# Performance work log

Hardware: AMD Instinct MI355X
Metric: run time of the kernel (lower is better)

Reference implementation:

```python
import jax, jax.numpy as jnp
import numpy as np
from jax import lax

K = 7            # neighborhood kernel size (odd)
HEADS = 6
DIM = 96
HID = int(DIM * 2.66)   # 255, Restormer-style hidden width


def _ln(x, w, b):
    # WithBias_LayerNorm over the channel axis (to_3d makes C the last dim)
    mu = x.mean(axis=1, keepdims=True)
    var = x.var(axis=1, keepdims=True)  # biased, matches unbiased=False
    return (x - mu) / jnp.sqrt(var + 1e-5) * w[None, :, None, None] + b[None, :, None, None]


def _conv1x1(x, w, b=None):
    y = jnp.einsum('bchw,oc->bohw', x, w)
    return y if b is None else y + b[None, :, None, None]


def _dwconv3x3(x, w, b=None):
    y = lax.conv_general_dilated(x, w, (1, 1), 'SAME',
                                 feature_group_count=x.shape[1],
                                 dimension_numbers=('NCHW', 'OIHW', 'NCHW'))
    return y if b is None else y + b[None, :, None, None]


def _l2norm(x):
    n = jnp.sqrt(jnp.sum(x * x, axis=-1, keepdims=True))
    return x / jnp.maximum(n, 1e-12)  # F.normalize semantics


def _na(x, qkv_w, qkv_b, qkv_dw_w, qkv_dw_b, rpb, temperature, proj_w, proj_b):
    # NeighborhoodAttention with edge-clamped K x K windows and RPB (dilation=1)
    B, C, H, W = x.shape
    hd = C // HEADS
    qkv = _dwconv3x3(_conv1x1(x, qkv_w, qkv_b), qkv_dw_w, qkv_dw_b)      # [B,3C,H,W]
    qkv = qkv.reshape(B, 3, HEADS, hd, H, W).transpose(1, 0, 2, 4, 5, 3)  # [3,B,h,H,W,d]
    q, k, v = _l2norm(qkv[0]), _l2norm(qkv[1]), qkv[2]
    off = K // 2
    ii = jnp.arange(H)
    jj = jnp.arange(W)
    ri = jnp.clip(ii - off, 0, H - K)[:, None] + jnp.arange(K)   # [H,K] neighbor rows
    cj = jnp.clip(jj - off, 0, W - K)[:, None] + jnp.arange(K)   # [W,K] neighbor cols
    bi = ii[:, None] - ri + (K - 1)   # rpb row idx in [0, 2K-2]
    bj = jj[:, None] - cj + (K - 1)
    RI = jnp.repeat(ri.T, K, axis=0)  # [K*K,H]; offset o=ki*K+kj -> ri[:,ki]
    CI = jnp.tile(cj.T, (K, 1))       # [K*K,W]; offset o        -> cj[:,kj]

    def qk_body(_, rc):
        r, c = rc
        kk = k[:, :, r][:, :, :, c]                       # [B,h,H,W,d] gathered keys
        return None, jnp.einsum('bhijd,bhijd->bhij', q, kk)

    _, scores = lax.scan(qk_body, None, (RI, CI))          # [K*K,B,h,H,W]
    attn = jnp.moveaxis(scores, 0, -1)                     # [B,h,H,W,K*K]
    bias = rpb[:, bi][..., bj]                             # [h,H,K,W,K]
    bias = bias.transpose(0, 1, 3, 2, 4).reshape(HEADS, H, W, K * K)
    attn = (attn + bias[None]) * temperature[None, :, None, None, None]
    attn = jax.nn.softmax(attn, axis=-1)

    def av_body(acc, inp):
        r, c, a = inp
        vv = v[:, :, r][:, :, :, c]                        # [B,h,H,W,d] gathered values
        return acc + a[..., None] * vv, None

    out, _ = lax.scan(av_body, jnp.zeros_like(v), (RI, CI, jnp.moveaxis(attn, -1, 0)))
    out = out.transpose(0, 1, 4, 2, 3).reshape(B, C, H, W)
    return _conv1x1(out, proj_w, proj_b)


def _ffn(x, pin_w, dw_w, pout_w):
    y = _dwconv3x3(_conv1x1(x, pin_w), dw_w)               # [B,2*HID,H,W]
    x1, x2 = jnp.split(y, 2, axis=1)
    return _conv1x1(jax.nn.gelu(x1, approximate=False) * x2, pout_w)


def setup_inputs():
    key = jax.random.key(0)
    ks = jax.random.split(key, 18)
    def rn(k, shape, s=0.05):
        return jax.random.normal(k, shape, jnp.float32) * s
    return {
        'x': jax.random.normal(ks[0], (4, DIM, 128, 128), jnp.float32),
        'ln1_w': 1.0 + rn(ks[1], (DIM,), 0.02), 'ln1_b': rn(ks[2], (DIM,), 0.02),
        'qkv_w': rn(ks[3], (3 * DIM, DIM)), 'qkv_b': rn(ks[4], (3 * DIM,), 0.01),
        'qkv_dw_w': rn(ks[5], (3 * DIM, 1, 3, 3)), 'qkv_dw_b': rn(ks[6], (3 * DIM,), 0.01),
        'rpb': rn(ks[7], (HEADS, 2 * K - 1, 2 * K - 1), 0.02),
        'temperature': jnp.ones((HEADS,), jnp.float32),
        'proj_w': rn(ks[8], (DIM, DIM)), 'proj_b': rn(ks[9], (DIM,), 0.01),
        'ln2_w': 1.0 + rn(ks[10], (DIM,), 0.02), 'ln2_b': rn(ks[11], (DIM,), 0.02),
        'pin_w': rn(ks[12], (2 * HID, DIM)),
        'dw_w': rn(ks[13], (2 * HID, 1, 3, 3)),
        'pout_w': rn(ks[14], (DIM, HID)),
        'beta': rn(ks[15], (DIM,), 0.1), 'gamma': rn(ks[16], (DIM,), 0.1),
    }


def reference(x, ln1_w, ln1_b, qkv_w, qkv_b, qkv_dw_w, qkv_dw_b, rpb, temperature,
              proj_w, proj_b, ln2_w, ln2_b, pin_w, dw_w, pout_w, beta, gamma):
    x = x + _na(_ln(x, ln1_w, ln1_b), qkv_w, qkv_b, qkv_dw_w, qkv_dw_b,
                rpb, temperature, proj_w, proj_b) * beta[None, :, None, None]
    x = x + _ffn(_ln(x, ln2_w, ln2_b), pin_w, dw_w, pout_w) * gamma[None, :, None, None]
    return x
```

## Files before the change

### kernel.cpp

```cpp
#include <hip/hip_runtime.h>
#include <math.h>

#define HT   128
#define WD   128
#define HW   16384
#define NB_B 4
#define BHW  65536
#define CD   96
#define C3   288
#define NH   6
#define HD   16
#define HID  255
#define HID2 510
#define KK   7
#define NNB  49

__global__ __launch_bounds__(256) void prep_weights(
    const float* __restrict__ qkv_w, const float* __restrict__ qkv_b,
    const float* __restrict__ ln1_w, const float* __restrict__ ln1_b,
    const float* __restrict__ pin_w, const float* __restrict__ ln2_w,
    const float* __restrict__ ln2_b,
    const float* __restrict__ proj_w, const float* __restrict__ pout_w,
    float* __restrict__ w1t, float* __restrict__ s1, float* __restrict__ b1,
    float* __restrict__ w2t, float* __restrict__ s2, float* __restrict__ b2,
    float* __restrict__ wpt, float* __restrict__ wot)
{
    int o = blockIdx.x * 256 + threadIdx.x;
    if (o < C3) {
        float s = 0.f, bb = qkv_b[o];
        for (int c = 0; c < CD; ++c) {
            float wv = qkv_w[o*CD+c] * ln1_w[c];
            w1t[(size_t)c * C3 + o] = wv;
            s += wv;
            bb += qkv_w[o*CD+c] * ln1_b[c];
        }
        s1[o] = s; b1[o] = bb;
    }
    if (o < HID2) {
        float s = 0.f, bb = 0.f;
        for (int c = 0; c < CD; ++c) {
            float wv = pin_w[o*CD+c] * ln2_w[c];
            w2t[(size_t)c * 512 + o] = wv;
            s += wv;
            bb += pin_w[o*CD+c] * ln2_b[c];
        }
        s2[o] = s; b2[o] = bb;
    } else if (o < 512) {
        for (int c = 0; c < CD; ++c) w2t[(size_t)c * 512 + o] = 0.f;
        s2[o] = 0.f; b2[o] = 0.f;
    }
    if (o < CD) {
        for (int c = 0; c < CD; ++c)
            wpt[(size_t)c * CD + o] = proj_w[o*CD + c];
        for (int c = 0; c < HID; ++c)
            wot[(size_t)c * CD + o] = pout_w[o*HID + c];
    }
}

__global__ __launch_bounds__(256) void ln_stats(
    const float* __restrict__ x, float* __restrict__ mu, float* __restrict__ rsig)
{
    int t  = blockIdx.x * 256 + threadIdx.x;
    int p4 = t * 4;
    int b = p4 >> 14, p = p4 & (HW - 1);
    const float* xp = x + (size_t)b * CD * HW + p;
    float4 s = {0.f,0.f,0.f,0.f}, s2 = {0.f,0.f,0.f,0.f};
    #pragma unroll 4
    for (int c = 0; c < CD; ++c) {
        float4 v = *(const float4*)(xp + (size_t)c * HW);
        s.x += v.x; s.y += v.y; s.z += v.z; s.w += v.w;
        s2.x = fmaf(v.x, v.x, s2.x); s2.y = fmaf(v.y, v.y, s2.y);
        s2.z = fmaf(v.z, v.z, s2.z); s2.w = fmaf(v.w, v.w, s2.w);
    }
    const float inv = 1.f / CD;
    float4 m, r;
    m.x = s.x*inv; m.y = s.y*inv; m.z = s.z*inv; m.w = s.w*inv;
    r.x = rsqrtf(s2.x*inv - m.x*m.x + 1e-5f);
    r.y = rsqrtf(s2.y*inv - m.y*m.y + 1e-5f);
    r.z = rsqrtf(s2.z*inv - m.z*m.z + 1e-5f);
    r.w = rsqrtf(s2.w*inv - m.w*m.w + 1e-5f);
    *(float4*)(mu + p4)   = m;
    *(float4*)(rsig + p4) = r;
}

template<int EPI>
__global__ __launch_bounds__(256) void conv1x1(
    const float* __restrict__ in, const float* __restrict__ wT,
    int Cin, int Cout, int OS,
    const float* __restrict__ S, const float* __restrict__ Bb,
    const float* __restrict__ mu, const float* __restrict__ rsig,
    const float* __restrict__ res, const float* __restrict__ scale,
    float* __restrict__ out)
{
    int t  = blockIdx.y * 256 + threadIdx.x;
    int p4 = t * 4;
    int o0 = blockIdx.x * 16;
    int b = p4 >> 14, p = p4 & (HW - 1);
    const float* ip = in + (size_t)b * Cin * HW + p;
    float4 acc[16];
    #pragma unroll
    for (int u = 0; u < 16; ++u) acc[u] = {0.f,0.f,0.f,0.f};
    #pragma unroll 2
    for (int c = 0; c < Cin; ++c) {
        float4 v = *(const float4*)(ip + (size_t)c * HW);
        const float* wr = wT + (size_t)c * OS + o0;
        #pragma unroll
        for (int u = 0; u < 16; ++u) {
            float wv = wr[u];
            acc[u].x = fmaf(v.x, wv, acc[u].x);
            acc[u].y = fmaf(v.y, wv, acc[u].y);
            acc[u].z = fmaf(v.z, wv, acc[u].z);
            acc[u].w = fmaf(v.w, wv, acc[u].w);
        }
    }
    size_t obase = (size_t)b * Cout * HW + p;
    if (EPI == 0) {
        float4 m = *(const float4*)(mu + p4);
        float4 r = *(const float4*)(rsig + p4);
        #pragma unroll
        for (int u = 0; u < 16; ++u) {
            int o = o0 + u;
            if (o < Cout) {
                float so = S[o], bo = Bb[o];
                float4 ov;
                ov.x = r.x * (acc[u].x - m.x * so) + bo;
                ov.y = r.y * (acc[u].y - m.y * so) + bo;
                ov.z = r.z * (acc[u].z - m.z * so) + bo;
                ov.w = r.w * (acc[u].w - m.w * so) + bo;
                *(float4*)(out + obase + (size_t)o * HW) = ov;
            }
        }
    } else if (EPI == 1) {
        #pragma unroll
        for (int u = 0; u < 16; ++u) {
            int o = o0 + u;
            float bo = Bb[o], sc = scale[o];
            float4 rv = *(const float4*)(res + obase + (size_t)o * HW);
            float4 ov;
            ov.x = rv.x + (acc[u].x + bo) * sc;
            ov.y = rv.y + (acc[u].y + bo) * sc;
            ov.z = rv.z + (acc[u].z + bo) * sc;
            ov.w = rv.w + (acc[u].w + bo) * sc;
            *(float4*)(out + obase + (size_t)o * HW) = ov;
        }
    } else {
        #pragma unroll
        for (int u = 0; u < 16; ++u) {
            int o = o0 + u;
            float sc = scale[o];
            float4 rv = *(const float4*)(res + obase + (size_t)o * HW);
            float4 ov;
            ov.x = rv.x + acc[u].x * sc;
            ov.y = rv.y + acc[u].y * sc;
            ov.z = rv.z + acc[u].z * sc;
            ov.w = rv.w + acc[u].w * sc;
            *(float4*)(out + obase + (size_t)o * HW) = ov;
        }
    }
}

__global__ __launch_bounds__(256) void dwconv_q(
    const float* __restrict__ in, const float* __restrict__ dwv,
    const float* __restrict__ bias, float* __restrict__ out)
{
    int t  = blockIdx.x * 256 + threadIdx.x;
    int p4 = t * 4;
    int bc = blockIdx.y;
    int b = bc / CD, c = bc % CD;
    int h = p4 >> 7, wx = p4 & (WD - 1);
    const float* ip = in + ((size_t)b * C3 + c) * HW;
    const float* wk = dwv + c * 9;
    float bz = bias[c];
    float a0 = bz, a1 = bz, a2 = bz, a3 = bz;
    #pragma unroll
    for (int ky = 0; ky < 3; ++ky) {
        int hh = h + ky - 1;
        if (hh < 0 || hh >= HT) continue;
        const float* rowp = ip + hh * WD + wx;
        float vm = (wx > 0)      ? rowp[-1] : 0.f;
        float4 v = *(const float4*)rowp;
        float vp = (wx + 4 < WD) ? rowp[4]  : 0.f;
        float w0 = wk[ky*3+0], w1 = wk[ky*3+1], w2 = wk[ky*3+2];
        a0 = fmaf(vm,  w0, a0); a0 = fmaf(v.x, w1, a0); a0 = fmaf(v.y, w2, a0);
        a1 = fmaf(v.x, w0, a1); a1 = fmaf(v.y, w1, a1); a1 = fmaf(v.z, w2, a1);
        a2 = fmaf(v.y, w0, a2); a2 = fmaf(v.z, w1, a2); a2 = fmaf(v.w, w2, a2);
        a3 = fmaf(v.z, w0, a3); a3 = fmaf(v.w, w1, a3); a3 = fmaf(vp,  w2, a3);
    }
    float4 ov; ov.x = a0; ov.y = a1; ov.z = a2; ov.w = a3;
    *(float4*)(out + ((size_t)b * CD + c) * HW + p4) = ov;
}

template<bool NORM>
__global__ __launch_bounds__(256) void dwconv_t(
    const float* __restrict__ in, const float* __restrict__ dwv,
    const float* __restrict__ bias, float* __restrict__ outt, int cbase)
{
    int t  = blockIdx.x * 256 + threadIdx.x;
    int p4 = t * 4;
    int bh = blockIdx.y;
    int b = bh / NH, head = bh % NH;
    int h = p4 >> 7, wx = p4 & (WD - 1);
    float4 acc[16];
    #pragma unroll
    for (int hd = 0; hd < 16; ++hd) {
        int c = cbase + head * HD + hd;
        const float* ip = in + ((size_t)b * C3 + c) * HW;
        const float* wk = dwv + c * 9;
        float bz = bias[c];
        float a0 = bz, a1 = bz, a2 = bz, a3 = bz;
        #pragma unroll
        for (int ky = 0; ky < 3; ++ky) {
            int hh = h + ky - 1;
            if (hh < 0 || hh >= HT) continue;
            const float* rowp = ip + hh * WD + wx;
            float vm = (wx > 0)      ? rowp[-1] : 0.f;
            float4 v = *(const float4*)rowp;
            float vp = (wx + 4 < WD) ? rowp[4]  : 0.f;
            float w0 = wk[ky*3+0], w1 = wk[ky*3+1], w2 = wk[ky*3+2];
            a0 = fmaf(vm,  w0, a0); a0 = fmaf(v.x, w1, a0); a0 = fmaf(v.y, w2, a0);
            a1 = fmaf(v.x, w0, a1); a1 = fmaf(v.y, w1, a1); a1 = fmaf(v.z, w2, a1);
            a2 = fmaf(v.y, w0, a2); a2 = fmaf(v.z, w1, a2); a2 = fmaf(v.w, w2, a2);
            a3 = fmaf(v.z, w0, a3); a3 = fmaf(v.w, w1, a3); a3 = fmaf(vp,  w2, a3);
        }
        acc[hd] = {a0, a1, a2, a3};
    }
    if (NORM) {
        float n0=0.f, n1=0.f, n2=0.f, n3=0.f;
        #pragma unroll
        for (int hd = 0; hd < 16; ++hd) {
            n0 = fmaf(acc[hd].x, acc[hd].x, n0);
            n1 = fmaf(acc[hd].y, acc[hd].y, n1);
            n2 = fmaf(acc[hd].z, acc[hd].z, n2);
            n3 = fmaf(acc[hd].w, acc[hd].w, n3);
        }
        n0 = 1.f / fmaxf(sqrtf(n0), 1e-12f);
        n1 = 1.f / fmaxf(sqrtf(n1), 1e-12f);
        n2 = 1.f / fmaxf(sqrtf(n2), 1e-12f);
        n3 = 1.f / fmaxf(sqrtf(n3), 1e-12f);
        #pragma unroll
        for (int hd = 0; hd < 16; ++hd) {
            acc[hd].x *= n0; acc[hd].y *= n1; acc[hd].z *= n2; acc[hd].w *= n3;
        }
    }
    float* op = outt + ((size_t)bh * HW + p4) * 16;
#define STORE_PX(pi, comp)                                                    \
    {                                                                         \
        float4 w0 = {acc[ 0].comp, acc[ 1].comp, acc[ 2].comp, acc[ 3].comp}; \
        float4 w1 = {acc[ 4].comp, acc[ 5].comp, acc[ 6].comp, acc[ 7].comp}; \
        float4 w2 = {acc[ 8].comp, acc[ 9].comp, acc[10].comp, acc[11].comp}; \
        float4 w3 = {acc[12].comp, acc[13].comp, acc[14].comp, acc[15].comp}; \
        *(float4*)(op + pi*16 +  0) = w0;                                     \
        *(float4*)(op + pi*16 +  4) = w1;                                     \
        *(float4*)(op + pi*16 +  8) = w2;                                     \
        *(float4*)(op + pi*16 + 12) = w3;                                     \
    }
    STORE_PX(0, x) STORE_PX(1, y) STORE_PX(2, z) STORE_PX(3, w)
#undef STORE_PX
}

__global__ __launch_bounds__(256) void dw_gate(
    const float* __restrict__ in, const float* __restrict__ dwv,
    float* __restrict__ out)
{
    int t  = blockIdx.x * 256 + threadIdx.x;
    int p4 = t * 4;
    int bj = blockIdx.y;
    int b = bj / HID, j = bj % HID;
    int h = p4 >> 7, wx = p4 & (WD - 1);
    const float* i1 = in + ((size_t)b * HID2 + j) * HW;
    const float* i2 = i1 + (size_t)HID * HW;
    const float* wk1 = dwv + j * 9;
    const float* wk2 = dwv + (j + HID) * 9;
    float a0=0.f,a1=0.f,a2=0.f,a3=0.f, g0=0.f,g1=0.f,g2=0.f,g3=0.f;
    #pragma unroll
    for (int ky = 0; ky < 3; ++ky) {
        int hh = h + ky - 1;
        if (hh < 0 || hh >= HT) continue;
        const float* r1 = i1 + hh * WD + wx;
        const float* r2 = i2 + hh * WD + wx;
        bool lm = (wx > 0), rp = (wx + 4 < WD);
        float um = lm ? r1[-1] : 0.f;
        float4 u = *(const float4*)r1;
        float up = rp ? r1[4] : 0.f;
        float vm = lm ? r2[-1] : 0.f;
        float4 v = *(const float4*)r2;
        float vp = rp ? r2[4] : 0.f;
        float w10 = wk1[ky*3+0], w11 = wk1[ky*3+1], w12 = wk1[ky*3+2];
        float w20 = wk2[ky*3+0], w21 = wk2[ky*3+1], w22 = wk2[ky*3+2];
        a0 = fmaf(um,  w10, a0); a0 = fmaf(u.x, w11, a0); a0 = fmaf(u.y, w12, a0);
        a1 = fmaf(u.x, w10, a1); a1 = fmaf(u.y, w11, a1); a1 = fmaf(u.z, w12, a1);
        a2 = fmaf(u.y, w10, a2); a2 = fmaf(u.z, w11, a2); a2 = fmaf(u.w, w12, a2);
        a3 = fmaf(u.z, w10, a3); a3 = fmaf(u.w, w11, a3); a3 = fmaf(up,  w12, a3);
        g0 = fmaf(vm,  w20, g0); g0 = fmaf(v.x, w21, g0); g0 = fmaf(v.y, w22, g0);
        g1 = fmaf(v.x, w20, g1); g1 = fmaf(v.y, w21, g1); g1 = fmaf(v.z, w22, g1);
        g2 = fmaf(v.y, w20, g2); g2 = fmaf(v.z, w21, g2); g2 = fmaf(v.w, w22, g2);
        g3 = fmaf(v.z, w20, g3); g3 = fmaf(v.w, w21, g3); g3 = fmaf(vp,  w22, g3);
    }
    const float is2 = 0.70710678118654752f;
    float4 ov;
    ov.x = 0.5f * a0 * (1.f + erff(a0 * is2)) * g0;
    ov.y = 0.5f * a1 * (1.f + erff(a1 * is2)) * g1;
    ov.z = 0.5f * a2 * (1.f + erff(a2 * is2)) * g2;
    ov.w = 0.5f * a3 * (1.f + erff(a3 * is2)) * g3;
    *(float4*)(out + ((size_t)b * HID + j) * HW + p4) = ov;
}

__global__ __launch_bounds__(256) void natten(
    const float* __restrict__ qd, const float* __restrict__ kt,
    const float* __restrict__ vt, const float* __restrict__ rpb,
    const float* __restrict__ temp, float* __restrict__ out)
{
    __shared__ float srpb[169];
    int bh = blockIdx.z;
    int b = bh / NH, head = bh % NH;
    float T = temp[head];
    if (threadIdx.x < 169) srpb[threadIdx.x] = rpb[head * 169 + threadIdx.x] * T;
    __syncthreads();

    int i = blockIdx.y * 16 + (threadIdx.x >> 4);
    int j = blockIdx.x * 16 + (threadIdx.x & 15);
    const float* qp  = qd + ((size_t)b * CD + head * HD) * HW + i * WD + j;
    const float* ktb = kt + (size_t)bh * HW * 16;
    const float* vtb = vt + (size_t)bh * HW * 16;

    float q[HD]; float qn = 0.f;
    #pragma unroll
    for (int d = 0; d < HD; ++d) { q[d] = qp[(size_t)d * HW]; qn = fmaf(q[d], q[d], qn); }
    qn = T / fmaxf(sqrtf(qn), 1e-12f);
    #pragma unroll
    for (int d = 0; d < HD; ++d) q[d] *= qn;

    int ri0 = min(max(i - 3, 0), HT - KK);
    int cj0 = min(max(j - 3, 0), WD - KK);
    int bi0 = i - ri0 + 6;
    int bj0 = j - cj0 + 6;

    float s[NNB]; float m = -1e30f;
    #pragma unroll
    for (int o = 0; o < NNB; ++o) {
        int r = ri0 + o / KK, c = cj0 + o % KK;
        const float4* kk = (const float4*)(ktb + ((size_t)(r * WD + c)) * 16);
        float4 k0 = kk[0], k1 = kk[1], k2 = kk[2], k3 = kk[3];
        float d0 = q[0]*k0.x + q[1]*k0.y + q[2]*k0.z + q[3]*k0.w;
        float d1 = q[4]*k1.x + q[5]*k1.y + q[6]*k1.z + q[7]*k1.w;
        float d2 = q[8]*k2.x + q[9]*k2.y + q[10]*k2.z + q[11]*k2.w;
        float d3 = q[12]*k3.x + q[13]*k3.y + q[14]*k3.z + q[15]*k3.w;
        float sv = (d0 + d1) + (d2 + d3)
                 + srpb[(bi0 - o / KK) * 13 + (bj0 - o % KK)];
        s[o] = sv;
        m = fmaxf(m, sv);
    }
    float l = 0.f;
    #pragma unroll
    for (int o = 0; o < NNB; ++o) { float pv = __expf(s[o] - m); s[o] = pv; l += pv; }
    float inv = 1.f / l;
    float ov[HD];
    #pragma unroll
    for (int d = 0; d < HD; ++d) ov[d] = 0.f;
    #pragma unroll
    for (int o = 0; o < NNB; ++o) {
        int r = ri0 + o / KK, c = cj0 + o % KK;
        const float4* vv = (const float4*)(vtb + ((size_t)(r * WD + c)) * 16);
        float4 v0 = vv[0], v1 = vv[1], v2 = vv[2], v3 = vv[3];
        float pv = s[o];
        ov[0]  = fmaf(pv, v0.x, ov[0]);  ov[1]  = fmaf(pv, v0.y, ov[1]);
        ov[2]  = fmaf(pv, v0.z, ov[2]);  ov[3]  = fmaf(pv, v0.w, ov[3]);
        ov[4]  = fmaf(pv, v1.x, ov[4]);  ov[5]  = fmaf(pv, v1.y, ov[5]);
        ov[6]  = fmaf(pv, v1.z, ov[6]);  ov[7]  = fmaf(pv, v1.w, ov[7]);
        ov[8]  = fmaf(pv, v2.x, ov[8]);  ov[9]  = fmaf(pv, v2.y, ov[9]);
        ov[10] = fmaf(pv, v2.z, ov[10]); ov[11] = fmaf(pv, v2.w, ov[11]);
        ov[12] = fmaf(pv, v3.x, ov[12]); ov[13] = fmaf(pv, v3.y, ov[13]);
        ov[14] = fmaf(pv, v3.z, ov[14]); ov[15] = fmaf(pv, v3.w, ov[15]);
    }
    float* op = out + ((size_t)b * CD + head * HD) * HW + i * WD + j;
    #pragma unroll
    for (int d = 0; d < HD; ++d) op[(size_t)d * HW] = ov[d] * inv;
}

extern "C" void kernel_launch(void* const* d_in, const int* in_sizes, int n_in,
                              void* d_out, int out_size, void* d_ws, size_t ws_size,
                              hipStream_t stream)
{
    const float* x        = (const float*)d_in[0];
    const float* ln1_w    = (const float*)d_in[1];
    const float* ln1_b    = (const float*)d_in[2];
    const float* qkv_w    = (const float*)d_in[3];
    const float* qkv_b    = (const float*)d_in[4];
    const float* qkv_dw_w = (const float*)d_in[5];
    const float* qkv_dw_b = (const float*)d_in[6];
    const float* rpb      = (const float*)d_in[7];
    const float* temp     = (const float*)d_in[8];
    const float* proj_w   = (const float*)d_in[9];
    const float* proj_b   = (const float*)d_in[10];
    const float* ln2_w    = (const float*)d_in[11];
    const float* ln2_b    = (const float*)d_in[12];
    const float* pin_w    = (const float*)d_in[13];
    const float* dw_w     = (const float*)d_in[14];
    const float* pout_w   = (const float*)d_in[15];
    const float* beta     = (const float*)d_in[16];
    const float* gamma    = (const float*)d_in[17];
    float* out = (float*)d_out;
    float* f   = (float*)d_ws;
    (void)in_sizes; (void)n_in; (void)out_size; (void)ws_size;

    float* W1T = f;
    float* W2T = W1T + 27648;
    float* WPT = W2T + 49152;
    float* WOT = WPT + 9216;
    float* S1  = WOT + 24480;
    float* B1  = S1 + 512;
    float* S2  = B1 + 512;
    float* B2  = S2 + 512;
    float* MU  = B2 + 512;
    float* RS  = MU + 65536;
    float* A   = f + 262144;
    float* QKV = A;
    float* QD  = A + 18874368;
    float* KT  = QD + 6291456;
    float* VT  = KT + 6291456;
    float* AO  = A + 37748736;
    float* X2  = A + 54460416;

    prep_weights<<<dim3(2), dim3(256), 0, stream>>>(
        qkv_w, qkv_b, ln1_w, ln1_b, pin_w, ln2_w, ln2_b, proj_w, pout_w,
        W1T, S1, B1, W2T, S2, B2, WPT, WOT);
    ln_stats<<<dim3(64), dim3(256), 0, stream>>>(x, MU, RS);
    conv1x1<0><<<dim3(18, 64), dim3(256), 0, stream>>>(
        x, W1T, CD, C3, C3, S1, B1, MU, RS, nullptr, nullptr, QKV);
    dwconv_q<<<dim3(16, NB_B * CD), dim3(256), 0, stream>>>(
        QKV, qkv_dw_w, qkv_dw_b, QD);
    dwconv_t<true><<<dim3(16, NB_B * NH), dim3(256), 0, stream>>>(
        QKV, qkv_dw_w, qkv_dw_b, KT, CD);
    dwconv_t<false><<<dim3(16, NB_B * NH), dim3(256), 0, stream>>>(
        QKV, qkv_dw_w, qkv_dw_b, VT, 2 * CD);
    natten<<<dim3(8, 8, NB_B * NH), dim3(256), 0, stream>>>(
        QD, KT, VT, rpb, temp, AO);
    conv1x1<1><<<dim3(6, 64), dim3(256), 0, stream>>>(
        AO, WPT, CD, CD, CD, nullptr, proj_b, nullptr, nullptr, x, beta, X2);
    ln_stats<<<dim3(64), dim3(256), 0, stream>>>(X2, MU, RS);
    conv1x1<0><<<dim3(32, 64), dim3(256), 0, stream>>>(
        X2, W2T, CD, HID2, 512, S2, B2, MU, RS, nullptr, nullptr, QKV);
    dw_gate<<<dim3(16, NB_B * HID), dim3(256), 0, stream>>>(QKV, dw_w, AO);
    conv1x1<2><<<dim3(6, 64), dim3(256), 0, stream>>>(
        AO, WOT, HID, CD, CD, nullptr, nullptr, nullptr, nullptr, X2, gamma, out);
}
```

Measured before the change: 650.8 us.

## Stage K/V halo tiles in shared memory for neighborhood attention

The natten kernel now cooperatively loads a 22x22 halo tile of keys, then of values, into LDS (padded stride 20 floats) and reads all 49 neighbours from shared memory instead of global/L2. Q is also written in pixel-major [B,h,HW,16] layout by reusing dwconv_t<false>, so each thread reads its query with four float4 loads. This removes roughly 49x redundant global gathers per pixel at the cost of about 39KB of LDS per block, which lowers occupancy, plus extra barriers between the K and V phases.

```diff
diff --git a/kernel.cpp b/kernel.cpp
--- a/kernel.cpp
+++ b/kernel.cpp
@@ -14,6 +14,9 @@
 #define HID2 510
 #define KK   7
 #define NNB  49
+#define LRD  22
+#define NFR  484
+#define FPAD 20
 
 __global__ __launch_bounds__(256) void prep_weights(
     const float* __restrict__ qkv_w, const float* __restrict__ qkv_b,
@@ -157,37 +160,6 @@
             *(float4*)(out + obase + (size_t)o * HW) = ov;
         }
     }
-}
-
-__global__ __launch_bounds__(256) void dwconv_q(
-    const float* __restrict__ in, const float* __restrict__ dwv,
-    const float* __restrict__ bias, float* __restrict__ out)
-{
-    int t  = blockIdx.x * 256 + threadIdx.x;
-    int p4 = t * 4;
-    int bc = blockIdx.y;
-    int b = bc / CD, c = bc % CD;
-    int h = p4 >> 7, wx = p4 & (WD - 1);
-    const float* ip = in + ((size_t)b * C3 + c) * HW;
-    const float* wk = dwv + c * 9;
-    float bz = bias[c];
-    float a0 = bz, a1 = bz, a2 = bz, a3 = bz;
-    #pragma unroll
-    for (int ky = 0; ky < 3; ++ky) {
-        int hh = h + ky - 1;
-        if (hh < 0 || hh >= HT) continue;
-        const float* rowp = ip + hh * WD + wx;
-        float vm = (wx > 0)      ? rowp[-1] : 0.f;
-        float4 v = *(const float4*)rowp;
-        float vp = (wx + 4 < WD) ? rowp[4]  : 0.f;
-        float w0 = wk[ky*3+0], w1 = wk[ky*3+1], w2 = wk[ky*3+2];
-        a0 = fmaf(vm,  w0, a0); a0 = fmaf(v.x, w1, a0); a0 = fmaf(v.y, w2, a0);
-        a1 = fmaf(v.x, w0, a1); a1 = fmaf(v.y, w1, a1); a1 = fmaf(v.z, w2, a1);
-        a2 = fmaf(v.y, w0, a2); a2 = fmaf(v.z, w1, a2); a2 = fmaf(v.w, w2, a2);
-        a3 = fmaf(v.z, w0, a3); a3 = fmaf(v.w, w1, a3); a3 = fmaf(vp,  w2, a3);
-    }
-    float4 ov; ov.x = a0; ov.y = a1; ov.z = a2; ov.w = a3;
-    *(float4*)(out + ((size_t)b * CD + c) * HW + p4) = ov;
 }
 
 template<bool NORM>
@@ -306,75 +278,122 @@
 }
 
 __global__ __launch_bounds__(256) void natten(
-    const float* __restrict__ qd, const float* __restrict__ kt,
+    const float* __restrict__ qt, const float* __restrict__ kt,
     const float* __restrict__ vt, const float* __restrict__ rpb,
     const float* __restrict__ temp, float* __restrict__ out)
 {
+    __shared__ __align__(16) float skv[NFR * FPAD];
     __shared__ float srpb[169];
     int bh = blockIdx.z;
     int b = bh / NH, head = bh % NH;
     float T = temp[head];
     if (threadIdx.x < 169) srpb[threadIdx.x] = rpb[head * 169 + threadIdx.x] * T;
-    __syncthreads();
-
-    int i = blockIdx.y * 16 + (threadIdx.x >> 4);
-    int j = blockIdx.x * 16 + (threadIdx.x & 15);
-    const float* qp  = qd + ((size_t)b * CD + head * HD) * HW + i * WD + j;
-    const float* ktb = kt + (size_t)bh * HW * 16;
-    const float* vtb = vt + (size_t)bh * HW * 16;
-
-    float q[HD]; float qn = 0.f;
-    #pragma unroll
-    for (int d = 0; d < HD; ++d) { q[d] = qp[(size_t)d * HW]; qn = fmaf(q[d], q[d], qn); }
+
+    int i0 = blockIdx.y * 16, j0 = blockIdx.x * 16;
+    int r0 = min(max(i0 - 3, 0), HT - LRD);
+    int c0 = min(max(j0 - 3, 0), WD - LRD);
+    const float4* ktb = (const float4*)(kt + (size_t)bh * HW * 16);
+    const float4* vtb = (const float4*)(vt + (size_t)bh * HW * 16);
+
+    #pragma unroll
+    for (int k = 0; k < 8; ++k) {
+        int g = threadIdx.x + k * 256;
+        if (g < NFR * 4) {
+            int fg = g >> 2, sub = g & 3;
+            int fr = fg / LRD, fc = fg - fr * LRD;
+            float4 v = ktb[(size_t)((r0 + fr) * WD + (c0 + fc)) * 4 + sub];
+            *(float4*)(&skv[fg * FPAD + sub * 4]) = v;
+        }
+    }
+
+    int i = i0 + (threadIdx.x >> 4);
+    int j = j0 + (threadIdx.x & 15);
+
+    const float* qp = qt + ((size_t)bh * HW + (size_t)(i * WD + j)) * 16;
+    float4 q0 = *(const float4*)(qp + 0);
+    float4 q1 = *(const float4*)(qp + 4);
+    float4 q2 = *(const float4*)(qp + 8);
+    float4 q3 = *(const float4*)(qp + 12);
+    float qn = 0.f;
+    qn = fmaf(q0.x,q0.x,qn); qn = fmaf(q0.y,q0.y,qn); qn = fmaf(q0.z,q0.z,qn); qn = fmaf(q0.w,q0.w,qn);
+    qn = fmaf(q1.x,q1.x,qn); qn = fmaf(q1.y,q1.y,qn); qn = fmaf(q1.z,q1.z,qn); qn = fmaf(q1.w,q1.w,qn);
+    qn = fmaf(q2.x,q2.x,qn); qn = fmaf(q2.y,q2.y,qn); qn = fmaf(q2.z,q2.z,qn); qn = fmaf(q2.w,q2.w,qn);
+    qn = fmaf(q3.x,q3.x,qn); qn = fmaf(q3.y,q3.y,qn); qn = fmaf(q3.z,q3.z,qn); qn = fmaf(q3.w,q3.w,qn);
     qn = T / fmaxf(sqrtf(qn), 1e-12f);
-    #pragma unroll
-    for (int d = 0; d < HD; ++d) q[d] *= qn;
+    q0.x*=qn; q0.y*=qn; q0.z*=qn; q0.w*=qn;
+    q1.x*=qn; q1.y*=qn; q1.z*=qn; q1.w*=qn;
+    q2.x*=qn; q2.y*=qn; q2.z*=qn; q2.w*=qn;
+    q3.x*=qn; q3.y*=qn; q3.z*=qn; q3.w*=qn;
 
     int ri0 = min(max(i - 3, 0), HT - KK);
     int cj0 = min(max(j - 3, 0), WD - KK);
-    int bi0 = i - ri0 + 6;
-    int bj0 = j - cj0 + 6;
+    int bi0 = i - ri0 + 6, bj0 = j - cj0 + 6;
+    const float* fb = &skv[((ri0 - r0) * LRD + (cj0 - c0)) * FPAD];
+
+    __syncthreads();
 
     float s[NNB]; float m = -1e30f;
     #pragma unroll
     for (int o = 0; o < NNB; ++o) {
-        int r = ri0 + o / KK, c = cj0 + o % KK;
-        const float4* kk = (const float4*)(ktb + ((size_t)(r * WD + c)) * 16);
-        float4 k0 = kk[0], k1 = kk[1], k2 = kk[2], k3 = kk[3];
-        float d0 = q[0]*k0.x + q[1]*k0.y + q[2]*k0.z + q[3]*k0.w;
-        float d1 = q[4]*k1.x + q[5]*k1.y + q[6]*k1.z + q[7]*k1.w;
-        float d2 = q[8]*k2.x + q[9]*k2.y + q[10]*k2.z + q[11]*k2.w;
-        float d3 = q[12]*k3.x + q[13]*k3.y + q[14]*k3.z + q[15]*k3.w;
-        float sv = (d0 + d1) + (d2 + d3)
-                 + srpb[(bi0 - o / KK) * 13 + (bj0 - o % KK)];
+        const float* kk = fb + ((o / KK) * LRD + (o % KK)) * FPAD;
+        float4 k0 = *(const float4*)(kk + 0);
+        float4 k1 = *(const float4*)(kk + 4);
+        float4 k2 = *(const float4*)(kk + 8);
+        float4 k3 = *(const float4*)(kk + 12);
+        float d = 0.f;
+        d = fmaf(q0.x,k0.x,d); d = fmaf(q0.y,k0.y,d); d = fmaf(q0.z,k0.z,d); d = fmaf(q0.w,k0.w,d);
+        d = fmaf(q1.x,k1.x,d); d = fmaf(q1.y,k1.y,d); d = fmaf(q1.z,k1.z,d); d = fmaf(q1.w,k1.w,d);
+        d = fmaf(q2.x,k2.x,d); d = fmaf(q2.y,k2.y,d); d = fmaf(q2.z,k2.z,d); d = fmaf(q2.w,k2.w,d);
+        d = fmaf(q3.x,k3.x,d); d = fmaf(q3.y,k3.y,d); d = fmaf(q3.z,k3.z,d); d = fmaf(q3.w,k3.w,d);
+        float sv = d + srpb[(bi0 - o / KK) * 13 + (bj0 - o % KK)];
         s[o] = sv;
         m = fmaxf(m, sv);
     }
+    __syncthreads();
+
+    #pragma unroll
+    for (int k = 0; k < 8; ++k) {
+        int g = threadIdx.x + k * 256;
+        if (g < NFR * 4) {
+            int fg = g >> 2, sub = g & 3;
+            int fr = fg / LRD, fc = fg - fr * LRD;
+            float4 v = vtb[(size_t)((r0 + fr) * WD + (c0 + fc)) * 4 + sub];
+            *(float4*)(&skv[fg * FPAD + sub * 4]) = v;
+        }
+    }
     float l = 0.f;
     #pragma unroll
     for (int o = 0; o < NNB; ++o) { float pv = __expf(s[o] - m); s[o] = pv; l += pv; }
     float inv = 1.f / l;
-    float ov[HD];
-    #pragma unroll
-    for (int d = 0; d < HD; ++d) ov[d] = 0.f;
+    __syncthreads();
+
+    float4 a0 = {0.f,0.f,0.f,0.f}, a1 = a0, a2 = a0, a3 = a0;
     #pragma unroll
     for (int o = 0; o < NNB; ++o) {
-        int r = ri0 + o / KK, c = cj0 + o % KK;
-        const float4* vv = (const float4*)(vtb + ((size_t)(r * WD + c)) * 16);
-        float4 v0 = vv[0], v1 = vv[1], v2 = vv[2], v3 = vv[3];
+        const float* vvp = fb + ((o / KK) * LRD + (o % KK)) * FPAD;
+        float4 v0 = *(const float4*)(vvp + 0);
+        float4 v1 = *(const float4*)(vvp + 4);
+        float4 v2 = *(const float4*)(vvp + 8);
+        float4 v3 = *(const float4*)(vvp + 12);
         float pv = s[o];
-        ov[0]  = fmaf(pv, v0.x, ov[0]);  ov[1]  = fmaf(pv, v0.y, ov[1]);
-        ov[2]  = fmaf(pv, v0.z, ov[2]);  ov[3]  = fmaf(pv, v0.w, ov[3]);
-        ov[4]  = fmaf(pv, v1.x, ov[4]);  ov[5]  = fmaf(pv, v1.y, ov[5]);
-        ov[6]  = fmaf(pv, v1.z, ov[6]);  ov[7]  = fmaf(pv, v1.w, ov[7]);
-        ov[8]  = fmaf(pv, v2.x, ov[8]);  ov[9]  = fmaf(pv, v2.y, ov[9]);
-        ov[10] = fmaf(pv, v2.z, ov[10]); ov[11] = fmaf(pv, v2.w, ov[11]);
-        ov[12] = fmaf(pv, v3.x, ov[12]); ov[13] = fmaf(pv, v3.y, ov[13]);
-        ov[14] = fmaf(pv, v3.z, ov[14]); ov[15] = fmaf(pv, v3.w, ov[15]);
+        a0.x = fmaf(pv, v0.x, a0.x); a0.y = fmaf(pv, v0.y, a0.y);
+        a0.z = fmaf(pv, v0.z, a0.z); a0.w = fmaf(pv, v0.w, a0.w);
+        a1.x = fmaf(pv, v1.x, a1.x); a1.y = fmaf(pv, v1.y, a1.y);
+        a1.z = fmaf(pv, v1.z, a1.z); a1.w = fmaf(pv, v1.w, a1.w);
+        a2.x = fmaf(pv, v2.x, a2.x); a2.y = fmaf(pv, v2.y, a2.y);
+        a2.z = fmaf(pv, v2.z, a2.z); a2.w = fmaf(pv, v2.w, a2.w);
+        a3.x = fmaf(pv, v3.x, a3.x); a3.y = fmaf(pv, v3.y, a3.y);
+        a3.z = fmaf(pv, v3.z, a3.z); a3.w = fmaf(pv, v3.w, a3.w);
     }
     float* op = out + ((size_t)b * CD + head * HD) * HW + i * WD + j;
-    #pragma unroll
-    for (int d = 0; d < HD; ++d) op[(size_t)d * HW] = ov[d] * inv;
+    op[(size_t) 0*HW] = a0.x*inv; op[(size_t) 1*HW] = a0.y*inv;
+    op[(size_t) 2*HW] = a0.z*inv; op[(size_t) 3*HW] = a0.w*inv;
+    op[(size_t) 4*HW] = a1.x*inv; op[(size_t) 5*HW] = a1.y*inv;
+    op[(size_t) 6*HW] = a1.z*inv; op[(size_t) 7*HW] = a1.w*inv;
+    op[(size_t) 8*HW] = a2.x*inv; op[(size_t) 9*HW] = a2.y*inv;
+    op[(size_t)10*HW] = a2.z*inv; op[(size_t)11*HW] = a2.w*inv;
+    op[(size_t)12*HW] = a3.x*inv; op[(size_t)13*HW] = a3.y*inv;
+    op[(size_t)14*HW] = a3.z*inv; op[(size_t)15*HW] = a3.w*inv;
 }
 
 extern "C" void kernel_launch(void* const* d_in, const int* in_sizes, int n_in,
@@ -415,8 +434,8 @@
     float* RS  = MU + 65536;
     float* A   = f + 262144;
     float* QKV = A;
-    float* QD  = A + 18874368;
-    float* KT  = QD + 6291456;
+    float* QT  = A + 18874368;
+    float* KT  = QT + 6291456;
     float* VT  = KT + 6291456;
     float* AO  = A + 37748736;
     float* X2  = A + 54460416;
@@ -427,14 +446,14 @@
     ln_stats<<<dim3(64), dim3(256), 0, stream>>>(x, MU, RS);
     conv1x1<0><<<dim3(18, 64), dim3(256), 0, stream>>>(
         x, W1T, CD, C3, C3, S1, B1, MU, RS, nullptr, nullptr, QKV);
-    dwconv_q<<<dim3(16, NB_B * CD), dim3(256), 0, stream>>>(
-        QKV, qkv_dw_w, qkv_dw_b, QD);
+    dwconv_t<false><<<dim3(16, NB_B * NH), dim3(256), 0, stream>>>(
+        QKV, qkv_dw_w, qkv_dw_b, QT, 0);
     dwconv_t<true><<<dim3(16, NB_B * NH), dim3(256), 0, stream>>>(
         QKV, qkv_dw_w, qkv_dw_b, KT, CD);
     dwconv_t<false><<<dim3(16, NB_B * NH), dim3(256), 0, stream>>>(
         QKV, qkv_dw_w, qkv_dw_b, VT, 2 * CD);
     natten<<<dim3(8, 8, NB_B * NH), dim3(256), 0, stream>>>(
-        QD, KT, VT, rpb, temp, AO);
+        QT, KT, VT, rpb, temp, AO);
     conv1x1<1><<<dim3(6, 64), dim3(256), 0, stream>>>(
         AO, WPT, CD, CD, CD, nullptr, proj_b, nullptr, nullptr, x, beta, X2);
     ln_stats<<<dim3(64), dim3(256), 0, stream>>>(X2, MU, RS);
```

Result: slower. 901.3 us (+38.5%).
